# Kernel optimization log

Hardware: AMD Instinct MI355X
Metric: run time of the kernel (lower is better)

Reference implementation:

```python
import jax, jax.numpy as jnp
import numpy as np

N, E, C, MID = 20000, 320000, 16, 32
EPS = 1e-8

# ---- real Clebsch-Gordan (Q_J) matrices for degree pairs up to l=1, real-SH m-order (-l..l) i.e. (y,z,x) for l=1 ----

def _q_matrices():
    Q0 = np.eye(3, dtype=np.float32)[:, :, None] / np.sqrt(3.0)          # 1x1 -> J=0
    eps = np.zeros((3, 3, 3), dtype=np.float32)
    for (a, b, c_) in [(0, 1, 2), (1, 2, 0), (2, 0, 1)]:
        eps[a, b, c_] = 1.0
        eps[a, c_, b] = -1.0
    Q1 = eps / np.sqrt(2.0)                                               # 1x1 -> J=1 (cross product)
    Q2 = np.zeros((3, 3, 5), dtype=np.float32)                            # 1x1 -> J=2 (sym traceless)
    s2 = 1.0 / np.sqrt(2.0); s6 = 1.0 / np.sqrt(6.0)
    Q2[2, 0, 0] = Q2[0, 2, 0] = s2          # ~xy
    Q2[0, 1, 1] = Q2[1, 0, 1] = s2          # ~yz
    Q2[0, 0, 2] = -s6; Q2[1, 1, 2] = 2 * s6; Q2[2, 2, 2] = -s6  # ~(2z2-x2-y2)
    Q2[1, 2, 3] = Q2[2, 1, 3] = s2          # ~xz
    Q2[2, 2, 4] = s2; Q2[0, 0, 4] = -s2     # ~(x2-y2)
    return Q0, Q1, Q2

_Q0, _Q1, _Q2 = _q_matrices()


def _basis(u):
    """u: [E,3] unit edge directions -> basis tensors per (d_in,d_out) pair."""
    x, y, z = u[:, 0], u[:, 1], u[:, 2]
    Ep = u.shape[0]
    Y0 = jnp.full((Ep,), 0.28209479177387814, u.dtype)
    Y1 = 0.4886025119029199 * jnp.stack([y, z, x], -1)                    # m=-1,0,1
    Y2 = jnp.stack([1.0925484305920792 * x * y,
                    1.0925484305920792 * y * z,
                    0.31539156525252005 * (3.0 * z * z - 1.0),
                    1.0925484305920792 * x * z,
                    0.5462742152960396 * (x * x - y * y)], -1)
    b00 = Y0.reshape(Ep, 1, 1, 1, 1, 1)
    b01 = Y1.reshape(Ep, 1, 3, 1, 1, 1)
    b10 = Y1.reshape(Ep, 1, 1, 1, 3, 1)
    K0 = Y0[:, None, None] * jnp.asarray(_Q0[:, :, 0])
    K1 = jnp.einsum('em,abm->eab', Y1, jnp.asarray(_Q1))
    K2 = jnp.einsum('em,abm->eab', Y2, jnp.asarray(_Q2))
    b11 = jnp.stack([K0, K1, K2], -1).reshape(Ep, 1, 3, 1, 3, 3)          # num_freq=3 (J=0,1,2)
    return b00, b01, b10, b11


def _bn(x, g, b):  # BatchNorm1d, training-mode stats over edges, eps=1e-5
    mu = x.mean(0)
    var = ((x - mu) ** 2).mean(0)
    return (x - mu) * jax.lax.rsqrt(var + 1e-5) * g + b


def _hidden(feat, W1, b1, g1, be1, W2, b2, g2, be2):
    h = jax.nn.relu(_bn(feat @ W1 + b1, g1, be1))
    return jax.nn.relu(_bn(h @ W2 + b2, g2, be2))


def _kernel(Rflat, basis, nco, do_dim, nci, di_dim, nf):
    # RadialFunc output view: [E, nc_out, 1, nc_in, 1, num_freq]; contract freq with basis
    R = Rflat.reshape(-1, nco, 1, nci, 1, nf)
    k = (R * basis).sum(-1)                        # [E,nco,do_dim,nci,di_dim]
    return k.reshape(-1, nco * do_dim, nci * di_dim)


def _norm_bias(x, bias):  # GNormBias: relu(|x| + b) * phase
    n = jnp.sqrt((x * x).sum(-1, keepdims=True) + 1e-12)
    phase = x / jnp.maximum(n, EPS)
    return jax.nn.relu(n[..., 0] + bias)[..., None] * phase


def _forward(src, dst, pos, c, v, w,
             rW1, rb1, rg1, rbe1, rW2, rb2, rg2, rbe2,
             w3_a00, b3_a00, w3_a01, b3_a01, w3_a10, b3_a10, w3_a11, b3_a11,
             w3_b01, b3_b01, w3_b11, b3_b11,
             selfA0, selfA1, selfB1, nbias0, nbias1):
    n_nodes = c.shape[0]
    n_edges = src.shape[0]
    rel = pos[dst] - pos[src]
    r = jnp.sqrt((rel * rel).sum(-1, keepdims=True))                      # [E,1]
    u = rel / jnp.maximum(r, EPS)
    b00, b01, b10, b11 = _basis(u)
    feat = jnp.concatenate([w, r], -1)                                    # [E, edge_dim+1]
    # all 6 radial-net hiddens at once: [6,E,MID]
    H = jax.vmap(_hidden, in_axes=(None, 0, 0, 0, 0, 0, 0, 0, 0))(
        feat, rW1, rb1, rg1, rbe1, rW2, rb2, rg2, rbe2)
    deg = jax.ops.segment_sum(jnp.ones((n_edges,), feat.dtype), dst, num_segments=n_nodes)
    inv = (1.0 / jnp.maximum(deg, 1.0))[:, None, None]
    mask = (deg > 0).astype(feat.dtype)[:, None, None]
    # ---- layer A: in {0:1,1:1} -> mid {0:C,1:C} ----
    k00 = _kernel(H[0] @ w3_a00 + b3_a00, b00, C, 1, 1, 1, 1)             # [E,C,1]
    k01 = _kernel(H[1] @ w3_a01 + b3_a01, b01, C, 3, 1, 1, 1)             # [E,3C,1]
    k10 = _kernel(H[2] @ w3_a10 + b3_a10, b10, C, 1, 1, 3, 1)             # [E,C,3]
    k11 = _kernel(H[3] @ w3_a11 + b3_a11, b11, C, 3, 1, 3, 3)             # [E,3C,3]
    s0 = c[src].reshape(n_edges, 1, 1)
    s1 = v[src].reshape(n_edges, 3, 1)
    m0 = (k00 @ s0 + k10 @ s1).reshape(n_edges, C, 1)
    m1 = (k01 @ s0 + k11 @ s1).reshape(n_edges, C, 3)
    h0 = jax.ops.segment_sum(m0, dst, num_segments=n_nodes) * inv \
         + jnp.einsum('oi,nid->nod', selfA0[0], c) * mask
    h1 = jax.ops.segment_sum(m1, dst, num_segments=n_nodes) * inv \
         + jnp.einsum('oi,nid->nod', selfA1[0], v) * mask
    # ---- GNormBias on mid fiber ----
    h0 = _norm_bias(h0, nbias0)
    h1 = _norm_bias(h1, nbias1)
    # ---- layer B: mid {0:C,1:C} -> out {1:2} ----
    kb01 = _kernel(H[4] @ w3_b01 + b3_b01, b01, 2, 3, C, 1, 1)            # [E,6,C]
    kb11 = _kernel(H[5] @ w3_b11 + b3_b11, b11, 2, 3, C, 3, 3)            # [E,6,3C]
    t0 = h0[src]                                                          # [E,C,1]
    t1 = h1[src].reshape(n_edges, C * 3, 1)
    mB = (kb01 @ t0 + kb11 @ t1).reshape(n_edges, 2, 3)
    out = jax.ops.segment_sum(mB, dst, num_segments=n_nodes) * inv \
          + jnp.einsum('oi,nid->nod', selfB1[0], h1) * mask
    return out                                                            # [N,2,3]


def setup_inputs() -> dict:
    key = jax.random.key(0)
    ks = jax.random.split(key, 40)
    def rn(i, shape, scale=1.0):
        return jax.random.normal(ks[i], shape, jnp.float32) * scale
    K = 6
    sc = 1.0 / np.sqrt(MID)
    d = {}
    d['src'] = jax.random.randint(ks[0], (E,), 0, N)
    d['dst'] = jax.random.randint(ks[1], (E,), 0, N)
    d['pos'] = rn(2, (N, 3))
    d['c'] = rn(3, (N, 1, 1))
    d['v'] = rn(4, (N, 1, 3))
    d['w'] = rn(5, (E, 1))
    d['rW1'] = rn(6, (K, 2, MID), 1.0 / np.sqrt(2.0))
    d['rb1'] = jnp.zeros((K, MID), jnp.float32)
    d['rg1'] = jnp.ones((K, MID), jnp.float32)
    d['rbe1'] = jnp.zeros((K, MID), jnp.float32)
    d['rW2'] = rn(7, (K, MID, MID), sc)
    d['rb2'] = jnp.zeros((K, MID), jnp.float32)
    d['rg2'] = jnp.ones((K, MID), jnp.float32)
    d['rbe2'] = jnp.zeros((K, MID), jnp.float32)
    d['w3_a00'] = rn(8, (MID, C), sc);      d['b3_a00'] = jnp.zeros((C,), jnp.float32)
    d['w3_a01'] = rn(9, (MID, C), sc);      d['b3_a01'] = jnp.zeros((C,), jnp.float32)
    d['w3_a10'] = rn(10, (MID, C), sc);     d['b3_a10'] = jnp.zeros((C,), jnp.float32)
    d['w3_a11'] = rn(11, (MID, 3 * C), sc); d['b3_a11'] = jnp.zeros((3 * C,), jnp.float32)
    d['w3_b01'] = rn(12, (MID, 2 * C), sc); d['b3_b01'] = jnp.zeros((2 * C,), jnp.float32)
    d['w3_b11'] = rn(13, (MID, 6 * C), sc); d['b3_b11'] = jnp.zeros((6 * C,), jnp.float32)
    d['selfA0'] = rn(14, (1, C, 1))
    d['selfA1'] = rn(15, (1, C, 1))
    d['selfB1'] = rn(16, (1, 2, C), 1.0 / np.sqrt(C))
    d['nbias0'] = rn(17, (C,))
    d['nbias1'] = rn(18, (C,))
    return d


def reference(src, dst, pos, c, v, w,
              rW1, rb1, rg1, rbe1, rW2, rb2, rg2, rbe2,
              w3_a00, b3_a00, w3_a01, b3_a01, w3_a10, b3_a10, w3_a11, b3_a11,
              w3_b01, b3_b01, w3_b11, b3_b11,
              selfA0, selfA1, selfB1, nbias0, nbias1):
    return _forward(src, dst, pos, c, v, w,
                    rW1, rb1, rg1, rbe1, rW2, rb2, rg2, rbe2,
                    w3_a00, b3_a00, w3_a01, b3_a01, w3_a10, b3_a10, w3_a11, b3_a11,
                    w3_b01, b3_b01, w3_b11, b3_b11,
                    selfA0, selfA1, selfB1, nbias0, nbias1)
```

## Files before the change

### kernel.cpp

```cpp
#include <hip/hip_runtime.h>

#define NN 20000
#define NE 320000
#define CDIM 16
#define MID 32
#define EPSF 1e-8f

#define SCHED_FENCE() __builtin_amdgcn_sched_barrier(0)

#define OFF_DEGI   848
#define ZERO_WORDS 20848
#define OFF_ROWPTR 20848
#define OFF_CURSOR 40864
#define OFF_EORDER 60864
#define OFF_SRCS   380864
#define OFF_WSRT   700864
#define OFF_FW1A   1020864
#define OFF_FW1B   1021056
#define OFF_FC1    1021248
#define OFF_BN2A   1021440
#define OFF_FC2    1021632
#define OFF_FW2T   1021824
#define OFF_ECS    1027968
#define OFF_H0N    2307968
#define OFF_H1N    2627968
#define OFF_MSGA0  3587968
#define OFF_MSGA1  8707968
#define OFF_MSGB   24067968

#define Y0C   0.28209479177387814f
#define Y1C   0.4886025119029199f
#define Y2C1  1.0925484305920792f
#define Y2C2  0.31539156525252005f
#define Y2C3  0.5462742152960396f
#define S2C   0.7071067811865476f
#define S6C   0.4082482904638631f
#define K0C   0.16286750396763996f

__device__ __forceinline__ void atomAddD(double* p, double v) {
  unsafeAtomicAdd(p, v);
}

__device__ __forceinline__ void mlpH_lds(
    const float* __restrict__ a1, const float* __restrict__ b1v,
    const float* __restrict__ c1, const float* __restrict__ c2,
    const float* __restrict__ W2T, float we, float r, float* H) {
  float h[MID];
#pragma unroll
  for (int j4 = 0; j4 < 8; ++j4) {
    float4 av = ((const float4*)a1)[j4];
    float4 bv = ((const float4*)b1v)[j4];
    float4 cv = ((const float4*)c1)[j4];
    h[4 * j4 + 0] = fmaxf(fmaf(we, av.x, fmaf(r, bv.x, cv.x)), 0.0f);
    h[4 * j4 + 1] = fmaxf(fmaf(we, av.y, fmaf(r, bv.y, cv.y)), 0.0f);
    h[4 * j4 + 2] = fmaxf(fmaf(we, av.z, fmaf(r, bv.z, cv.z)), 0.0f);
    h[4 * j4 + 3] = fmaxf(fmaf(we, av.w, fmaf(r, bv.w, cv.w)), 0.0f);
  }
  SCHED_FENCE();
#pragma unroll
  for (int jg = 0; jg < 8; ++jg) {
#pragma unroll
    for (int jq = 0; jq < 4; ++jq) {
      const int j = jg * 4 + jq;
      float acc = c2[j];
      const float4* wp = (const float4*)(W2T + j * MID);
#pragma unroll
      for (int i4 = 0; i4 < 8; ++i4) {
        float4 wv = wp[i4];
        acc = fmaf(h[4 * i4 + 0], wv.x, acc);
        acc = fmaf(h[4 * i4 + 1], wv.y, acc);
        acc = fmaf(h[4 * i4 + 2], wv.z, acc);
        acc = fmaf(h[4 * i4 + 3], wv.w, acc);
      }
// ... 29 lines not shown
  for (int jg = 0; jg < 8; ++jg) {
#pragma unroll
    for (int jq = 0; jq < 4; ++jq) {
      const int j = jg * 4 + jq;
      float c2v = c2[j];
      float accA = c2v, accB = c2v;
      const float4* wp = (const float4*)(W2T + j * MID);
#pragma unroll
      for (int i4 = 0; i4 < 8; ++i4) {
        float4 wv = wp[i4];
        accA = fmaf(hA[4 * i4 + 0], wv.x, accA);
        accB = fmaf(hB[4 * i4 + 0], wv.x, accB);
        accA = fmaf(hA[4 * i4 + 1], wv.y, accA);
        accB = fmaf(hB[4 * i4 + 1], wv.y, accB);
        accA = fmaf(hA[4 * i4 + 2], wv.z, accA);
        accB = fmaf(hB[4 * i4 + 2], wv.z, accB);
        accA = fmaf(hA[4 * i4 + 3], wv.w, accA);
        accB = fmaf(hB[4 * i4 + 3], wv.w, accB);
      }
      HA[j] = fmaxf(accA, 0.0f);
      HB[j] = fmaxf(accB, 0.0f);
    }
    SCHED_FENCE();
  }
}

__global__ __launch_bounds__(256) void k_hist(
    const int* __restrict__ dst, float* __restrict__ ws) {
  int e = blockIdx.x * blockDim.x + threadIdx.x;
  if (e >= NE) return;
  atomicAdd((int*)ws + OFF_DEGI + dst[e], 1);
}

__global__ void k_scan(float* __restrict__ ws) {
  __shared__ int buf[256];
  __shared__ int carry;
  const int* degi = (const int*)ws + OFF_DEGI;
  int* rowptr = (int*)ws + OFF_ROWPTR;
  int* cursor = (int*)ws + OFF_CURSOR;
  int tid = threadIdx.x;
  if (tid == 0) carry = 0;
  __syncthreads();
  for (int base = 0; base < NN; base += 256) {
    int v = (base + tid < NN) ? degi[base + tid] : 0;
    buf[tid] = v;
    __syncthreads();
    for (int off = 1; off < 256; off <<= 1) {
      int t = buf[tid];
      int add = (tid >= off) ? buf[tid - off] : 0;
      __syncthreads();
      buf[tid] = t + add;
      __syncthreads();
    }
    int excl = buf[tid] - v;
    if (base + tid < NN) {
      rowptr[base + tid] = carry + excl;
      cursor[base + tid] = carry + excl;
    }
    __syncthreads();
    if (tid == 255) carry += buf[255];
    __syncthreads();
  }
  if (tid == 0) rowptr[NN] = carry;
}

__global__ __launch_bounds__(256) void k_scatter(
    const int* __restrict__ dst, float* __restrict__ ws) {
  int e = blockIdx.x * blockDim.x + threadIdx.x;
  if (e >= NE) return;
  int* cursor = (int*)ws + OFF_CURSOR;
  int* eorder = (int*)ws + OFF_EORDER;
  int d = dst[e];
  int p = atomicAdd(cursor + d, 1);
  eorder[p] = e;
}

__global__ __launch_bounds__(256) void k_geo(
    const int* __restrict__ src, const int* __restrict__ dst,
    const float* __restrict__ pos, const float* __restrict__ w,
    float* __restrict__ ws) {
  __shared__ double sred[20];
  double lw = 0, lr = 0, lww = 0, lrr = 0, lwr = 0;
  const int* eorder = (const int*)ws + OFF_EORDER;
  int* srcs = (int*)ws + OFF_SRCS;
  float* wsrt = ws + OFF_WSRT;
  float4* ecs = (float4*)(ws + OFF_ECS);
  for (int t = blockIdx.x * blockDim.x + threadIdx.x; t < NE;
       t += gridDim.x * blockDim.x) {
    int e = eorder[t];
    int s = src[e], d = dst[e];
    float dx = pos[3 * d + 0] - pos[3 * s + 0];
    float dy = pos[3 * d + 1] - pos[3 * s + 1];
    float dz = pos[3 * d + 2] - pos[3 * s + 2];
    float r = sqrtf(dx * dx + dy * dy + dz * dz);
    float ri = 1.0f / fmaxf(r, EPSF);
    ecs[t] = make_float4(r, dx * ri, dy * ri, dz * ri);
    float we = w[e];
    wsrt[t] = we;
    srcs[t] = s;
    double wd = (double)we, rd = (double)r;
    lw += wd; lr += rd; lww += wd * wd; lrr += rd * rd; lwr += wd * rd;
  }
#pragma unroll
  for (int d = 32; d >= 1; d >>= 1) {
    lw += __shfl_xor(lw, d);
    lr += __shfl_xor(lr, d);
    lww += __shfl_xor(lww, d);
    lrr += __shfl_xor(lrr, d);
    lwr += __shfl_xor(lwr, d);
  }
  int wid = threadIdx.x >> 6;
  if ((threadIdx.x & 63) == 0) {
    sred[0 * 4 + wid] = lw;
    sred[1 * 4 + wid] = lr;
    sred[2 * 4 + wid] = lww;
    sred[3 * 4 + wid] = lrr;
    sred[4 * 4 + wid] = lwr;
  }
  __syncthreads();
  if (threadIdx.x < 5) {
    double v = sred[threadIdx.x * 4 + 0] + sred[threadIdx.x * 4 + 1]
             + sred[threadIdx.x * 4 + 2] + sred[threadIdx.x * 4 + 3];
    atomAddD((double*)ws + threadIdx.x * 8, v);
  }
}

__global__ void k_fin1(const float* __restrict__ rW1, const float* __restrict__ rb1,
                       const float* __restrict__ rg1, const float* __restrict__ rbe1,
                       float* __restrict__ ws) {
  int t = threadIdx.x;
  int k = t >> 5, j = t & 31;
  const double* s1 = (const double*)ws;
  double Sw = s1[0], Sr = s1[8], Sww = s1[16], Srr = s1[24], Swr = s1[32];
  const double inv = 1.0 / (double)NE;
  double W0 = (double)rW1[k * 64 + j], W1 = (double)rW1[k * 64 + 32 + j];
  double b = (double)rb1[k * 32 + j];
  double mlin = (Sw * W0 + Sr * W1) * inv;
  double mu = mlin + b;
  double ex2 = (Sww * W0 * W0 + Srr * W1 * W1 + 2.0 * Swr * W0 * W1) * inv
             + 2.0 * b * mlin + b * b;
  double var = ex2 - mu * mu;
  double a = (double)rg1[k * 32 + j] / sqrt(var + 1e-5);
  ws[OFF_FW1A + t] = (float)(W0 * a);
  ws[OFF_FW1B + t] = (float)(W1 * a);
  ws[OFF_FC1 + t] = (float)((double)rbe1[k * 32 + j] - mlin * a);
}

__global__ __launch_bounds__(256) void k_stats2(
    const float* __restrict__ rW2, const float* __restrict__ rb2,
    float* __restrict__ ws) {
  const int k = blockIdx.y;
  const int j0 = blockIdx.z * 16;
  __shared__ __align__(16) float sW1a[32], sW1b[32], sc1[32];
  __shared__ __align__(16) float sW2c[512];
  __shared__ float sb2[16];
  __shared__ float sredf[2][16][4];
  int tid = threadIdx.x;
  if (tid < 32) {
    sW1a[tid] = ws[OFF_FW1A + k * 32 + tid];
    sW1b[tid] = ws[OFF_FW1B + k * 32 + tid];
    sc1[tid] = ws[OFF_FC1 + k * 32 + tid];
  }
  if (tid < 16) sb2[tid] = rb2[k * 32 + j0 + tid];
  for (int t = tid; t < 512; t += 256) {
    int jj = t >> 5, i = t & 31;
    sW2c[t] = rW2[k * 1024 + i * 32 + j0 + jj];
  }
  __syncthreads();
  const float4* ecs = (const float4*)(ws + OFF_ECS);
  const float* wsrt = ws + OFF_WSRT;
  float lsum[16], lsq[16];
#pragma unroll
  for (int jj = 0; jj < 16; ++jj) { lsum[jj] = 0.0f; lsq[jj] = 0.0f; }
  const int NP = NE / 2;
  for (int p = blockIdx.x * blockDim.x + tid; p < NP;
       p += gridDim.x * blockDim.x) {
    int e0 = 2 * p;
    float r0 = ecs[e0].x, r1 = ecs[e0 + 1].x;
    float w0 = wsrt[e0], w1 = wsrt[e0 + 1];
    float h0[MID], h1[MID];
#pragma unroll
    for (int j4 = 0; j4 < 8; ++j4) {
      float4 av = ((const float4*)sW1a)[j4];
      float4 bv = ((const float4*)sW1b)[j4];
      float4 cv = ((const float4*)sc1)[j4];
      h0[4 * j4 + 0] = fmaxf(fmaf(w0, av.x, fmaf(r0, bv.x, cv.x)), 0.0f);
      h1[4 * j4 + 0] = fmaxf(fmaf(w1, av.x, fmaf(r1, bv.x, cv.x)), 0.0f);
      h0[4 * j4 + 1] = fmaxf(fmaf(w0, av.y, fmaf(r0, bv.y, cv.y)), 0.0f);
      h1[4 * j4 + 1] = fmaxf(fmaf(w1, av.y, fmaf(r1, bv.y, cv.y)), 0.0f);
      h0[4 * j4 + 2] = fmaxf(fmaf(w0, av.z, fmaf(r0, bv.z, cv.z)), 0.0f);
      h1[4 * j4 + 2] = fmaxf(fmaf(w1, av.z, fmaf(r1, bv.z, cv.z)), 0.0f);
      h0[4 * j4 + 3] = fmaxf(fmaf(w0, av.w, fmaf(r0, bv.w, cv.w)), 0.0f);
      h1[4 * j4 + 3] = fmaxf(fmaf(w1, av.w, fmaf(r1, bv.w, cv.w)), 0.0f);
    }
    SCHED_FENCE();
#pragma unroll
    for (int jg = 0; jg < 4; ++jg) {
#pragma unroll
      for (int jq = 0; jq < 4; ++jq) {
        const int jj = jg * 4 + jq;
        float aE0 = sb2[jj], aE1 = sb2[jj];
        const float4* wp = (const float4*)(sW2c + jj * 32);
#pragma unroll
        for (int i4 = 0; i4 < 8; ++i4) {
          float4 wv = wp[i4];
          aE0 = fmaf(h0[4 * i4 + 0], wv.x, aE0);
          aE1 = fmaf(h1[4 * i4 + 0], wv.x, aE1);
          aE0 = fmaf(h0[4 * i4 + 1], wv.y, aE0);
          aE1 = fmaf(h1[4 * i4 + 1], wv.y, aE1);
          aE0 = fmaf(h0[4 * i4 + 2], wv.z, aE0);
          aE1 = fmaf(h1[4 * i4 + 2], wv.z, aE1);
          aE0 = fmaf(h0[4 * i4 + 3], wv.w, aE0);
// ... 24 lines not shown
    int jj = tid & 15, which = tid >> 4;
    float v = sredf[which][jj][0] + sredf[which][jj][1]
            + sredf[which][jj][2] + sredf[which][jj][3];
    double* s2 = (double*)(ws + 80);
    atomAddD(s2 + k * 64 + which * 32 + j0 + jj, (double)v);
  }
}

__global__ void k_fin2(const float* __restrict__ rb2,
                       const float* __restrict__ rg2, const float* __restrict__ rbe2,
                       float* __restrict__ ws) {
  int t = threadIdx.x;
  int k = t >> 5, j = t & 31;
  const double* s2 = (const double*)(ws + 80);
  const double inv = 1.0 / (double)NE;
  double mu = s2[k * 64 + j] * inv;
  double ex2 = s2[k * 64 + 32 + j] * inv;
  double var = ex2 - mu * mu;
  double a = (double)rg2[t] / sqrt(var + 1e-5);
  ws[OFF_BN2A + t] = (float)a;
  ws[OFF_FC2 + t] = (float)((double)rbe2[t] + ((double)rb2[t] - mu) * a);
}

__global__ __launch_bounds__(256) void k_fold2(const float* __restrict__ rW2,
                                               float* __restrict__ ws) {
  int idx = blockIdx.x * blockDim.x + threadIdx.x;
  if (idx >= 6144) return;
  int k = idx >> 10, rem = idx & 1023;
  int j = rem >> 5, i = rem & 31;
  ws[OFF_FW2T + idx] = rW2[k * 1024 + i * 32 + j] * ws[OFF_BN2A + k * 32 + j];
}

__global__ __launch_bounds__(256) void k_passA0(
    const float* __restrict__ cI, const float* __restrict__ vI,
    const float* __restrict__ w00, const float* __restrict__ b00,
    const float* __restrict__ w10, const float* __restrict__ b10,
    float* __restrict__ ws) {
  __shared__ __align__(16) float sW1a[64], sW1b[64], sc1[64], sc2[64];
  __shared__ __align__(16) float sW2T[2048];
  __shared__ __align__(16) float sP00[512], sP10[512];
  __shared__ float sB00[16], sB10[16];
  int tid = threadIdx.x;
  if (tid < 32) {
    sW1a[tid] = ws[OFF_FW1A + tid];       sW1a[32 + tid] = ws[OFF_FW1A + 64 + tid];
    sW1b[tid] = ws[OFF_FW1B + tid];       sW1b[32 + tid] = ws[OFF_FW1B + 64 + tid];
    sc1[tid]  = ws[OFF_FC1 + tid];        sc1[32 + tid]  = ws[OFF_FC1 + 64 + tid];
    sc2[tid]  = ws[OFF_FC2 + tid];        sc2[32 + tid]  = ws[OFF_FC2 + 64 + tid];
  }
  for (int t = tid; t < 2048; t += 256) {
    sW2T[t] = ws[OFF_FW2T + ((t < 1024) ? t : (1024 + t))];
  }
  for (int t = tid; t < 512; t += 256) {
    int i = t >> 4, co = t & 15;
    sP00[co * 32 + i] = w00[t];
    sP10[co * 32 + i] = w10[t];
  }
  if (tid < 16) { sB00[tid] = b00[tid]; sB10[tid] = b10[tid]; }
  __syncthreads();

  const int* srcs = (const int*)ws + OFF_SRCS;
  const float* wsrt = ws + OFF_WSRT;
  const float4* ecs = (const float4*)(ws + OFF_ECS);
  int t = blockIdx.x * blockDim.x + tid;
  if (t >= NE) return;
  int s = srcs[t];
  float4 E = ecs[t];
  float we = wsrt[t];
  float cs = cI[s];
  float v0 = vI[3 * s + 0], v1 = vI[3 * s + 1], v2 = vI[3 * s + 2];
  float dY1v = Y1C * (E.z * v0 + E.w * v1 + E.y * v2);

  float H[MID], m0[CDIM];
  mlpH_lds(sW1a, sW1b, sc1, sc2, sW2T, we, E.x, H);
  float f0 = Y0C * cs;
#pragma unroll
  for (int cg = 0; cg < 4; ++cg) {
#pragma unroll
    for (int cq = 0; cq < 4; ++cq) {
      const int co = cg * 4 + cq;
      float a = sB00[co];
      const float4* wp = (const float4*)(sP00 + co * 32);
#pragma unroll
      for (int i4 = 0; i4 < 8; ++i4) {
        float4 wv = wp[i4];
        a = fmaf(H[4 * i4 + 0], wv.x, a);
        a = fmaf(H[4 * i4 + 1], wv.y, a);
        a = fmaf(H[4 * i4 + 2], wv.z, a);
        a = fmaf(H[4 * i4 + 3], wv.w, a);
      }
      m0[co] = a * f0;
    }
    SCHED_FENCE();
  }
  mlpH_lds(sW1a + 32, sW1b + 32, sc1 + 32, sc2 + 32, sW2T + 1024, we, E.x, H);
#pragma unroll
  for (int cg = 0; cg < 4; ++cg) {
#pragma unroll
    for (int cq = 0; cq < 4; ++cq) {
      const int co = cg * 4 + cq;
      float a = sB10[co];
      const float4* wp = (const float4*)(sP10 + co * 32);
#pragma unroll
      for (int i4 = 0; i4 < 8; ++i4) {
        float4 wv = wp[i4];
        a = fmaf(H[4 * i4 + 0], wv.x, a);
        a = fmaf(H[4 * i4 + 1], wv.y, a);
        a = fmaf(H[4 * i4 + 2], wv.z, a);
        a = fmaf(H[4 * i4 + 3], wv.w, a);
      }
      m0[co] = fmaf(a, dY1v, m0[co]);
    }
    SCHED_FENCE();
  }
  float4* mp = (float4*)(ws + OFF_MSGA0) + t * 4;
#pragma unroll
  for (int q = 0; q < 4; ++q)
    mp[q] = make_float4(m0[4 * q], m0[4 * q + 1], m0[4 * q + 2], m0[4 * q + 3]);
}

__global__ __launch_bounds__(256) void k_passA1(
    const float* __restrict__ cI, const float* __restrict__ vI,
    const float* __restrict__ w01, const float* __restrict__ b01,
    const float* __restrict__ w11, const float* __restrict__ b11,
    float* __restrict__ ws) {
  __shared__ __align__(16) float sW1a[64], sW1b[64], sc1[64], sc2[64];
  __shared__ __align__(16) float sW2T[2048];
  __shared__ __align__(16) float sP01[512], sP11[1536];
  __shared__ float sB01[16], sB11[48];
  int tid = threadIdx.x;
  if (tid < 32) {
    sW1a[tid] = ws[OFF_FW1A + 32 + tid];  sW1a[32 + tid] = ws[OFF_FW1A + 96 + tid];
    sW1b[tid] = ws[OFF_FW1B + 32 + tid];  sW1b[32 + tid] = ws[OFF_FW1B + 96 + tid];
    sc1[tid]  = ws[OFF_FC1 + 32 + tid];   sc1[32 + tid]  = ws[OFF_FC1 + 96 + tid];
    sc2[tid]  = ws[OFF_FC2 + 32 + tid];   sc2[32 + tid]  = ws[OFF_FC2 + 96 + tid];
  }
  for (int t = tid; t < 1024; t += 256) {
    sW2T[t] = ws[OFF_FW2T + 1024 + t];
    sW2T[1024 + t] = ws[OFF_FW2T + 3072 + t];
  }
  for (int t = tid; t < 512; t += 256) {
    int i = t >> 4, co = t & 15;
    sP01[co * 32 + i] = w01[t];
  }
  for (int t = tid; t < 1536; t += 256) {
    int i = t / 48, c = t - i * 48;
    sP11[c * 32 + i] = w11[t];
  }
  if (tid < 16) sB01[tid] = b01[tid];
  if (tid < 48) sB11[tid] = b11[tid];
  __syncthreads();

  const int* srcs = (const int*)ws + OFF_SRCS;
  const float* wsrt = ws + OFF_WSRT;
  const float4* ecs = (const float4*)(ws + OFF_ECS);
  int t = blockIdx.x * blockDim.x + tid;
  if (t >= NE) return;
  int s = srcs[t];
  float4 E = ecs[t];
  float we = wsrt[t];
  float cs = cI[s];

  float H[MID];
  float ra[16];
  mlpH_lds(sW1a, sW1b, sc1, sc2, sW2T, we, E.x, H);
#pragma unroll
  for (int cg = 0; cg < 4; ++cg) {
#pragma unroll
    for (int cq = 0; cq < 4; ++cq) {
      const int co = cg * 4 + cq;
      float a = sB01[co];
      const float4* wp = (const float4*)(sP01 + co * 32);
#pragma unroll
      for (int i4 = 0; i4 < 8; ++i4) {
        float4 wv = wp[i4];
        a = fmaf(H[4 * i4 + 0], wv.x, a);
        a = fmaf(H[4 * i4 + 1], wv.y, a);
        a = fmaf(H[4 * i4 + 2], wv.z, a);
        a = fmaf(H[4 * i4 + 3], wv.w, a);
      }
      ra[co] = a;
    }
    SCHED_FENCE();
  }
  mlpH_lds(sW1a + 32, sW1b + 32, sc1 + 32, sc2 + 32, sW2T + 1024, we, E.x, H);
  float y10 = Y1C * E.z, y11 = Y1C * E.w, y12 = Y1C * E.y;
  float KV[3][3];
  {
    float ux = E.y, uy = E.z, uz = E.w;
    float y20 = Y2C1 * ux * uy, y21 = Y2C1 * uy * uz;
    float y22 = Y2C2 * (3.0f * uz * uz - 1.0f);
    float y23 = Y2C1 * ux * uz, y24 = Y2C3 * (ux * ux - uy * uy);
    float S00 = -S6C * y22 - S2C * y24;
    float S11 = 2.0f * S6C * y22;
    float S22 = -S6C * y22 + S2C * y24;
    float S01 = S2C * y21, S02 = S2C * y20, S12 = S2C * y23;
    float v0 = vI[3 * s + 0], v1 = vI[3 * s + 1], v2 = vI[3 * s + 2];
    KV[0][0] = K0C * v0; KV[0][1] = K0C * v1; KV[0][2] = K0C * v2;
    KV[1][0] = S2C * (y12 * v1 - y11 * v2);
    KV[1][1] = S2C * (y10 * v2 - y12 * v0);
    KV[1][2] = S2C * (y11 * v0 - y10 * v1);
    KV[2][0] = S00 * v0 + S01 * v1 + S02 * v2;
    KV[2][1] = S01 * v0 + S11 * v1 + S12 * v2;
    KV[2][2] = S02 * v0 + S12 * v1 + S22 * v2;
  }
  float cy0 = cs * y10, cy1 = cs * y11, cy2 = cs * y12;
#pragma unroll 1
  for (int g = 0; g < 4; ++g) {
    float a[12];
#pragma unroll
    for (int q = 0; q < 4; ++q) {
      int co = g * 4 + q;
      float R0 = sB11[co * 3 + 0], R1 = sB11[co * 3 + 1], R2 = sB11[co * 3 + 2];
      const float4* p0 = (const float4*)(sP11 + (co * 3 + 0) * 32);
      const float4* p1 = (const float4*)(sP11 + (co * 3 + 1) * 32);
      const float4* p2 = (const float4*)(sP11 + (co * 3 + 2) * 32);
#pragma unroll
      for (int i4 = 0; i4 < 8; ++i4) {
        float4 w0v = p0[i4], w1v = p1[i4], w2v = p2[i4];
        float h0 = H[4 * i4 + 0], h1 = H[4 * i4 + 1];
        float h2 = H[4 * i4 + 2], h3 = H[4 * i4 + 3];
        R0 = fmaf(h0, w0v.x, R0); R1 = fmaf(h0, w1v.x, R1); R2 = fmaf(h0, w2v.x, R2);
        R0 = fmaf(h1, w0v.y, R0); R1 = fmaf(h1, w1v.y, R1); R2 = fmaf(h1, w2v.y, R2);
        R0 = fmaf(h2, w0v.z, R0); R1 = fmaf(h2, w1v.z, R1); R2 = fmaf(h2, w2v.z, R2);
        R0 = fmaf(h3, w0v.w, R0); R1 = fmaf(h3, w1v.w, R1); R2 = fmaf(h3, w2v.w, R2);
      }
      float r_ = ra[co];
      a[q * 3 + 0] = fmaf(r_, cy0, R0 * KV[0][0] + R1 * KV[1][0] + R2 * KV[2][0]);
      a[q * 3 + 1] = fmaf(r_, cy1, R0 * KV[0][1] + R1 * KV[1][1] + R2 * KV[2][1]);
      a[q * 3 + 2] = fmaf(r_, cy2, R0 * KV[0][2] + R1 * KV[1][2] + R2 * KV[2][2]);
    }
    float4* mp = (float4*)(ws + OFF_MSGA1 + g * (NE * 12)) + t * 3;
    mp[0] = make_float4(a[0], a[1], a[2], a[3]);
    mp[1] = make_float4(a[4], a[5], a[6], a[7]);
    mp[2] = make_float4(a[8], a[9], a[10], a[11]);
    SCHED_FENCE();
  }
}

__global__ __launch_bounds__(256) void k_nodeA(
    const float* __restrict__ cI, const float* __restrict__ vI,
    const float* __restrict__ selfA0, const float* __restrict__ selfA1,
    const float* __restrict__ nbias0, const float* __restrict__ nbias1,
    float* __restrict__ ws) {
  int idx = blockIdx.x * blockDim.x + threadIdx.x;
  if (idx >= NN * CDIM) return;
  int n = idx >> 4, co = idx & 15;
  const int* rowptr = (const int*)ws + OFF_ROWPTR;
  int r0 = rowptr[n], r1 = rowptr[n + 1];
  const float* mA0 = ws + OFF_MSGA0;
  const float* mA1 = ws + OFF_MSGA1 + (co >> 2) * (NE * 12) + (co & 3) * 3;
  float x0 = 0.0f, xa = 0.0f, xb = 0.0f, xc = 0.0f;
  for (int row = r0; row < r1; ++row) {
    x0 += mA0[row * 16 + co];
    xa += mA1[row * 12 + 0];
    xb += mA1[row * 12 + 1];
    xc += mA1[row * 12 + 2];
  }
  float dg = (float)(r1 - r0);
  float iv = 1.0f / fmaxf(dg, 1.0f);
  float mk = dg > 0.0f ? 1.0f : 0.0f;
  x0 = x0 * iv + selfA0[co] * cI[n] * mk;
  float n0 = sqrtf(x0 * x0 + 1e-12f);
  ws[OFF_H0N + idx] = fmaxf(n0 + nbias0[co], 0.0f) * (x0 / fmaxf(n0, EPSF));
  xa = xa * iv + selfA1[co] * vI[3 * n + 0] * mk;
  xb = xb * iv + selfA1[co] * vI[3 * n + 1] * mk;
  xc = xc * iv + selfA1[co] * vI[3 * n + 2] * mk;
  float nv = sqrtf(xa * xa + xb * xb + xc * xc + 1e-12f);
  float sc = fmaxf(nv + nbias1[co], 0.0f) / fmaxf(nv, EPSF);
  ws[OFF_H1N + idx * 3 + 0] = xa * sc;
  ws[OFF_H1N + idx * 3 + 1] = xb * sc;
  ws[OFF_H1N + idx * 3 + 2] = xc * sc;
}

__global__ __launch_bounds__(256) void k_passB(
    const float* __restrict__ wb01, const float* __restrict__ bb01,
    const float* __restrict__ wb11, const float* __restrict__ bb11,
    float* __restrict__ ws) {
  __shared__ __align__(16) float sW1a[64], sW1b[64], sc1[64], sc2[64];
  __shared__ __align__(16) float sW2T[2048];
  __shared__ __align__(16) float sPB01[1024];
  __shared__ __align__(16) float sPB11[3072];
  __shared__ float sBB01[32];
  __shared__ float sBB11[96];
  int tid = threadIdx.x;
  if (tid < 64) {
    sW1a[tid] = ws[OFF_FW1A + 128 + tid];
    sW1b[tid] = ws[OFF_FW1B + 128 + tid];
    sc1[tid] = ws[OFF_FC1 + 128 + tid];
    sc2[tid] = ws[OFF_FC2 + 128 + tid];
  }
  for (int t = tid; t < 2048; t += 256) sW2T[t] = ws[OFF_FW2T + 4096 + t];
  for (int t = tid; t < 1024; t += 256) {
    int i = t >> 5, c = t & 31;
    int o = c >> 4, ci = c & 15;
    sPB01[(ci * 2 + o) * 32 + i] = wb01[t];
  }
  for (int t = tid; t < 3072; t += 256) {
    int i = t / 96, c = t - i * 96;
    int o = c / 48, rem = c - o * 48;
    int ci = rem / 3, f = rem - ci * 3;
    sPB11[(ci * 6 + o * 3 + f) * 32 + i] = wb11[t];
  }
  if (tid < 32) {
    int o = tid >> 4, ci = tid & 15;
    sBB01[ci * 2 + o] = bb01[tid];
  }
  if (tid < 96) {
    int o = tid / 48, rem = tid - o * 48;
    int ci = rem / 3, f = rem - ci * 3;
    sBB11[ci * 6 + o * 3 + f] = bb11[tid];
  }
  __syncthreads();

  const int* srcs = (const int*)ws + OFF_SRCS;
  const float* wsrt = ws + OFF_WSRT;
  const float4* ecs = (const float4*)(ws + OFF_ECS);
  const int NP = NE / 2;
  int p = blockIdx.x * blockDim.x + tid;
  if (p >= NP) return;
  {
    int tA = 2 * p, tB = 2 * p + 1;
    int sA = srcs[tA], sB_ = srcs[tB];
    float4 EA = ecs[tA], EB = ecs[tB];
    float weA = wsrt[tA], weB = wsrt[tB];

    float HA[MID], HB[MID];
    mlpH2_lds(sW1a, sW1b, sc1, sc2, sW2T, weA, EA.x, weB, EB.x, HA, HB);
    const float* h0pA = ws + OFF_H0N + sA * CDIM;
    const float* h0pB = ws + OFF_H0N + sB_ * CDIM;
    float A0A = 0.0f, A1A = 0.0f, A0B = 0.0f, A1B = 0.0f;
#pragma unroll 1
    for (int ci = 0; ci < CDIM; ++ci) {
      float bA = h0pA[ci], bB = h0pB[ci];
      float R0A = sBB01[ci * 2 + 0], R1A = sBB01[ci * 2 + 1];
      float R0B = R0A, R1B = R1A;
      const float4* p0 = (const float4*)(sPB01 + (ci * 2 + 0) * 32);
      const float4* p1 = (const float4*)(sPB01 + (ci * 2 + 1) * 32);
#pragma unroll
      for (int i4 = 0; i4 < 8; ++i4) {
        float4 w0v = p0[i4], w1v = p1[i4];
        float hA0 = HA[4 * i4 + 0], hB0 = HB[4 * i4 + 0];
        float hA1 = HA[4 * i4 + 1], hB1 = HB[4 * i4 + 1];
        float hA2 = HA[4 * i4 + 2], hB2 = HB[4 * i4 + 2];
        float hA3 = HA[4 * i4 + 3], hB3 = HB[4 * i4 + 3];
        R0A = fmaf(hA0, w0v.x, R0A); R0B = fmaf(hB0, w0v.x, R0B);
        R1A = fmaf(hA0, w1v.x, R1A); R1B = fmaf(hB0, w1v.x, R1B);
        R0A = fmaf(hA1, w0v.y, R0A); R0B = fmaf(hB1, w0v.y, R0B);
        R1A = fmaf(hA1, w1v.y, R1A); R1B = fmaf(hB1, w1v.y, R1B);
        R0A = fmaf(hA2, w0v.z, R0A); R0B = fmaf(hB2, w0v.z, R0B);
        R1A = fmaf(hA2, w1v.z, R1A); R1B = fmaf(hB2, w1v.z, R1B);
        R0A = fmaf(hA3, w0v.w, R0A); R0B = fmaf(hB3, w0v.w, R0B);
        R1A = fmaf(hA3, w1v.w, R1A); R1B = fmaf(hB3, w1v.w, R1B);
      }
      A0A = fmaf(R0A, bA, A0A); A1A = fmaf(R1A, bA, A1A);
      A0B = fmaf(R0B, bB, A0B); A1B = fmaf(R1B, bB, A1B);
      SCHED_FENCE();
    }
// ... 17 lines not shown
        float RB = RA;
        const float4* wp = (const float4*)(sPB11 + (ci * 6 + of) * 32);
#pragma unroll
        for (int i4 = 0; i4 < 8; ++i4) {
          float4 wv = wp[i4];
          RA = fmaf(HA[4 * i4 + 0], wv.x, RA);
          RB = fmaf(HB[4 * i4 + 0], wv.x, RB);
          RA = fmaf(HA[4 * i4 + 1], wv.y, RA);
          RB = fmaf(HB[4 * i4 + 1], wv.y, RB);
          RA = fmaf(HA[4 * i4 + 2], wv.z, RA);
          RB = fmaf(HB[4 * i4 + 2], wv.z, RB);
          RA = fmaf(HA[4 * i4 + 3], wv.w, RA);
          RB = fmaf(HB[4 * i4 + 3], wv.w, RB);
        }
        GA[of][0] = fmaf(RA, bA0, GA[of][0]);
        GA[of][1] = fmaf(RA, bA1, GA[of][1]);
        GA[of][2] = fmaf(RA, bA2, GA[of][2]);
        GB[of][0] = fmaf(RB, bB0, GB[of][0]);
        GB[of][1] = fmaf(RB, bB1, GB[of][1]);
        GB[of][2] = fmaf(RB, bB2, GB[of][2]);
      }
      SCHED_FENCE();
    }
    {
      float ux = EA.y, uy = EA.z, uz = EA.w;
      float y10 = Y1C * uy, y11 = Y1C * uz, y12 = Y1C * ux;
      float y20 = Y2C1 * ux * uy, y21 = Y2C1 * uy * uz;
      float y22 = Y2C2 * (3.0f * uz * uz - 1.0f);
      float y23 = Y2C1 * ux * uz, y24 = Y2C3 * (ux * ux - uy * uy);
      float S00 = -S6C * y22 - S2C * y24;
      float S11 = 2.0f * S6C * y22;
      float S22 = -S6C * y22 + S2C * y24;
      float S01 = S2C * y21, S02 = S2C * y20, S12 = S2C * y23;
      float4* mp = (float4*)(ws + OFF_MSGB) + tA * 2;
#pragma unroll
      for (int o = 0; o < 2; ++o) {
        float Ao = (o == 0) ? A0A : A1A;
        float m0 = Ao * y10 + K0C * GA[o * 3 + 0][0]
                 + S2C * (y12 * GA[o * 3 + 1][1] - y11 * GA[o * 3 + 1][2])
                 + S00 * GA[o * 3 + 2][0] + S01 * GA[o * 3 + 2][1] + S02 * GA[o * 3 + 2][2];
        float m1 = Ao * y11 + K0C * GA[o * 3 + 0][1]
                 + S2C * (y10 * GA[o * 3 + 1][2] - y12 * GA[o * 3 + 1][0])
                 + S01 * GA[o * 3 + 2][0] + S11 * GA[o * 3 + 2][1] + S12 * GA[o * 3 + 2][2];
        float m2 = Ao * y12 + K0C * GA[o * 3 + 0][2]
                 + S2C * (y11 * GA[o * 3 + 1][0] - y10 * GA[o * 3 + 1][1])
                 + S02 * GA[o * 3 + 2][0] + S12 * GA[o * 3 + 2][1] + S22 * GA[o * 3 + 2][2];
        mp[o] = make_float4(m0, m1, m2, 0.0f);
      }
    }
    {
      float ux = EB.y, uy = EB.z, uz = EB.w;
      float y10 = Y1C * uy, y11 = Y1C * uz, y12 = Y1C * ux;
      float y20 = Y2C1 * ux * uy, y21 = Y2C1 * uy * uz;
      float y22 = Y2C2 * (3.0f * uz * uz - 1.0f);
      float y23 = Y2C1 * ux * uz, y24 = Y2C3 * (ux * ux - uy * uy);
      float S00 = -S6C * y22 - S2C * y24;
      float S11 = 2.0f * S6C * y22;
      float S22 = -S6C * y22 + S2C * y24;
      float S01 = S2C * y21, S02 = S2C * y20, S12 = S2C * y23;
      float4* mp = (float4*)(ws + OFF_MSGB) + tB * 2;
#pragma unroll
      for (int o = 0; o < 2; ++o) {
        float Ao = (o == 0) ? A0B : A1B;
        float m0 = Ao * y10 + K0C * GB[o * 3 + 0][0]
                 + S2C * (y12 * GB[o * 3 + 1][1] - y11 * GB[o * 3 + 1][2])
                 + S00 * GB[o * 3 + 2][0] + S01 * GB[o * 3 + 2][1] + S02 * GB[o * 3 + 2][2];
        float m1 = Ao * y11 + K0C * GB[o * 3 + 0][1]
                 + S2C * (y10 * GB[o * 3 + 1][2] - y12 * GB[o * 3 + 1][0])
                 + S01 * GB[o * 3 + 2][0] + S11 * GB[o * 3 + 2][1] + S12 * GB[o * 3 + 2][2];
        float m2 = Ao * y12 + K0C * GB[o * 3 + 0][2]
                 + S2C * (y11 * GB[o * 3 + 1][0] - y10 * GB[o * 3 + 1][1])
                 + S02 * GB[o * 3 + 2][0] + S12 * GB[o * 3 + 2][1] + S22 * GB[o * 3 + 2][2];
        mp[o] = make_float4(m0, m1, m2, 0.0f);
      }
    }
  }
}

__global__ __launch_bounds__(256) void k_nodeB(
    const float* __restrict__ selfB1, float* __restrict__ out,
    const float* __restrict__ ws) {
  int idx = blockIdx.x * blockDim.x + threadIdx.x;
  if (idx >= NN * 6) return;
  int n = idx / 6;
  int q = idx - n * 6;
  int o = q / 3, a = q - o * 3;
  const int* rowptr = (const int*)ws + OFF_ROWPTR;
  int r0 = rowptr[n], r1 = rowptr[n + 1];
  const float* msgB = ws + OFF_MSGB;
  int col = o * 4 + a;
  float sum = 0.0f;
  for (int row = r0; row < r1; ++row) sum += msgB[row * 8 + col];
  float dg = (float)(r1 - r0);
  float iv = 1.0f / fmaxf(dg, 1.0f);
  float mk = dg > 0.0f ? 1.0f : 0.0f;
  const float* h1p = ws + OFF_H1N + n * CDIM * 3;
  float self = 0.0f;
#pragma unroll
  for (int ci = 0; ci < CDIM; ++ci)
    self = fmaf(selfB1[o * CDIM + ci], h1p[ci * 3 + a], self);
  out[idx] = sum * iv + self * mk;
}

extern "C" void kernel_launch(void* const* d_in, const int* in_sizes, int n_in,
                              void* d_out, int out_size, void* d_ws, size_t ws_size,
                              hipStream_t stream) {
  (void)in_sizes; (void)n_in; (void)out_size; (void)ws_size;
  const int* src = (const int*)d_in[0];
  const int* dst = (const int*)d_in[1];
  const float* pos = (const float*)d_in[2];
  const float* cI = (const float*)d_in[3];
  const float* vI = (const float*)d_in[4];
  const float* w = (const float*)d_in[5];
  const float* rW1 = (const float*)d_in[6];
  const float* rb1 = (const float*)d_in[7];
  const float* rg1 = (const float*)d_in[8];
  const float* rbe1 = (const float*)d_in[9];
  const float* rW2 = (const float*)d_in[10];
  const float* rb2 = (const float*)d_in[11];
  const float* rg2 = (const float*)d_in[12];
  const float* rbe2 = (const float*)d_in[13];
  const float* w3_a00 = (const float*)d_in[14];
  const float* b3_a00 = (const float*)d_in[15];
  const float* w3_a01 = (const float*)d_in[16];
  const float* b3_a01 = (const float*)d_in[17];
  const float* w3_a10 = (const float*)d_in[18];
  const float* b3_a10 = (const float*)d_in[19];
  const float* w3_a11 = (const float*)d_in[20];
  const float* b3_a11 = (const float*)d_in[21];
  const float* w3_b01 = (const float*)d_in[22];
  const float* b3_b01 = (const float*)d_in[23];
  const float* w3_b11 = (const float*)d_in[24];
  const float* b3_b11 = (const float*)d_in[25];
  const float* selfA0 = (const float*)d_in[26];
  const float* selfA1 = (const float*)d_in[27];
  const float* selfB1 = (const float*)d_in[28];
  const float* nbias0 = (const float*)d_in[29];
  const float* nbias1 = (const float*)d_in[30];
  float* ws = (float*)d_ws;
  float* out = (float*)d_out;

  hipMemsetAsync(d_ws, 0, (size_t)ZERO_WORDS * 4, stream);

  k_hist<<<1250, 256, 0, stream>>>(dst, ws);
  k_scan<<<1, 256, 0, stream>>>(ws);
  k_scatter<<<1250, 256, 0, stream>>>(dst, ws);
  k_geo<<<1250, 256, 0, stream>>>(src, dst, pos, w, ws);
  k_fin1<<<1, 192, 0, stream>>>(rW1, rb1, rg1, rbe1, ws);
  k_stats2<<<dim3(256, 6, 2), 256, 0, stream>>>(rW2, rb2, ws);
  k_fin2<<<1, 192, 0, stream>>>(rb2, rg2, rbe2, ws);
  k_fold2<<<24, 256, 0, stream>>>(rW2, ws);
  k_passA0<<<1250, 256, 0, stream>>>(cI, vI, w3_a00, b3_a00, w3_a10, b3_a10, ws);
  k_passA1<<<1250, 256, 0, stream>>>(cI, vI, w3_a01, b3_a01, w3_a11, b3_a11, ws);
  k_nodeA<<<1250, 256, 0, stream>>>(cI, vI, selfA0, selfA1, nbias0, nbias1, ws);
  k_passB<<<625, 256, 0, stream>>>(w3_b01, b3_b01, w3_b11, b3_b11, ws);
  k_nodeB<<<469, 256, 0, stream>>>(selfB1, out, ws);
}
```

Baseline: 540.2 us.

## Replace CSR sort and per-edge message buffers with atomic scatter-add into node accumulators

Drops the scan and scatter kernels that sorted edges by destination, along with the per-edge message arrays that the node kernels later gathered over CSR rows. Edge kernels now read src, dst and w directly in original order and atomically add their messages into per-node float accumulators, which the node kernels read directly. This removes two launches, the permutation traffic and large intermediate writes. In exchange it adds many float atomics, contended on high-degree nodes, a larger memset, and a nondeterministic summation order.

Result: slower. 1.480 ms (+173.9%).

```diff
diff --git a/kernel.cpp b/kernel.cpp
--- a/kernel.cpp
+++ b/kernel.cpp
@@ -9,24 +9,19 @@
 #define SCHED_FENCE() __builtin_amdgcn_sched_barrier(0)
 
 #define OFF_DEGI   848
-#define ZERO_WORDS 20848
-#define OFF_ROWPTR 20848
-#define OFF_CURSOR 40864
-#define OFF_EORDER 60864
-#define OFF_SRCS   380864
-#define OFF_WSRT   700864
-#define OFF_FW1A   1020864
-#define OFF_FW1B   1021056
-#define OFF_FC1    1021248
-#define OFF_BN2A   1021440
-#define OFF_FC2    1021632
-#define OFF_FW2T   1021824
-#define OFF_ECS    1027968
-#define OFF_H0N    2307968
-#define OFF_H1N    2627968
-#define OFF_MSGA0  3587968
-#define OFF_MSGA1  8707968
-#define OFF_MSGB   24067968
+#define OFF_ACCA0  20848
+#define OFF_ACCA1  340848
+#define OFF_ACCB   1300848
+#define ZERO_WORDS 1420848
+#define OFF_FW1A   1420848
+#define OFF_FW1B   1421040
+#define OFF_FC1    1421232
+#define OFF_BN2A   1421424
+#define OFF_FC2    1421616
+#define OFF_FW2T   1421808
+#define OFF_ECS    1427952
+#define OFF_H0N    2707952
+#define OFF_H1N    3027952
 
 #define Y0C   0.28209479177387814f
 #define Y1C   0.4886025119029199f
@@ -39,6 +34,9 @@
 
 __device__ __forceinline__ void atomAddD(double* p, double v) {
   unsafeAtomicAdd(p, v);
+}
+__device__ __forceinline__ void atomAddF(float* p, float v) {
+  atomicAdd(p, v);
 }
 
 __device__ __forceinline__ void mlpH_lds(
@@ -134,72 +132,23 @@
   atomicAdd((int*)ws + OFF_DEGI + dst[e], 1);
 }
 
-__global__ void k_scan(float* __restrict__ ws) {
-  __shared__ int buf[256];
-  __shared__ int carry;
-  const int* degi = (const int*)ws + OFF_DEGI;
-  int* rowptr = (int*)ws + OFF_ROWPTR;
-  int* cursor = (int*)ws + OFF_CURSOR;
-  int tid = threadIdx.x;
-  if (tid == 0) carry = 0;
-  __syncthreads();
-  for (int base = 0; base < NN; base += 256) {
-    int v = (base + tid < NN) ? degi[base + tid] : 0;
-    buf[tid] = v;
-    __syncthreads();
-    for (int off = 1; off < 256; off <<= 1) {
-      int t = buf[tid];
-      int add = (tid >= off) ? buf[tid - off] : 0;
-      __syncthreads();
-      buf[tid] = t + add;
-      __syncthreads();
-    }
-    int excl = buf[tid] - v;
-    if (base + tid < NN) {
-      rowptr[base + tid] = carry + excl;
-      cursor[base + tid] = carry + excl;
-    }
-    __syncthreads();
-    if (tid == 255) carry += buf[255];
-    __syncthreads();
-  }
-  if (tid == 0) rowptr[NN] = carry;
-}
-
-__global__ __launch_bounds__(256) void k_scatter(
-    const int* __restrict__ dst, float* __restrict__ ws) {
-  int e = blockIdx.x * blockDim.x + threadIdx.x;
-  if (e >= NE) return;
-  int* cursor = (int*)ws + OFF_CURSOR;
-  int* eorder = (int*)ws + OFF_EORDER;
-  int d = dst[e];
-  int p = atomicAdd(cursor + d, 1);
-  eorder[p] = e;
-}
-
 __global__ __launch_bounds__(256) void k_geo(
     const int* __restrict__ src, const int* __restrict__ dst,
     const float* __restrict__ pos, const float* __restrict__ w,
     float* __restrict__ ws) {
   __shared__ double sred[20];
   double lw = 0, lr = 0, lww = 0, lrr = 0, lwr = 0;
-  const int* eorder = (const int*)ws + OFF_EORDER;
-  int* srcs = (int*)ws + OFF_SRCS;
-  float* wsrt = ws + OFF_WSRT;
   float4* ecs = (float4*)(ws + OFF_ECS);
-  for (int t = blockIdx.x * blockDim.x + threadIdx.x; t < NE;
-       t += gridDim.x * blockDim.x) {
-    int e = eorder[t];
+  for (int e = blockIdx.x * blockDim.x + threadIdx.x; e < NE;
+       e += gridDim.x * blockDim.x) {
     int s = src[e], d = dst[e];
     float dx = pos[3 * d + 0] - pos[3 * s + 0];
     float dy = pos[3 * d + 1] - pos[3 * s + 1];
     float dz = pos[3 * d + 2] - pos[3 * s + 2];
     float r = sqrtf(dx * dx + dy * dy + dz * dz);
     float ri = 1.0f / fmaxf(r, EPSF);
-    ecs[t] = make_float4(r, dx * ri, dy * ri, dz * ri);
+    ecs[e] = make_float4(r, dx * ri, dy * ri, dz * ri);
     float we = w[e];
-    wsrt[t] = we;
-    srcs[t] = s;
     double wd = (double)we, rd = (double)r;
     lw += wd; lr += rd; lww += wd * wd; lrr += rd * rd; lwr += wd * rd;
   }
@@ -250,7 +199,7 @@
 
 __global__ __launch_bounds__(256) void k_stats2(
     const float* __restrict__ rW2, const float* __restrict__ rb2,
-    float* __restrict__ ws) {
+    const float* __restrict__ w, float* __restrict__ ws) {
   const int k = blockIdx.y;
   const int j0 = blockIdx.z * 16;
   __shared__ __align__(16) float sW1a[32], sW1b[32], sc1[32];
@@ -270,7 +219,6 @@
   }
   __syncthreads();
   const float4* ecs = (const float4*)(ws + OFF_ECS);
-  const float* wsrt = ws + OFF_WSRT;
   float lsum[16], lsq[16];
 #pragma unroll
   for (int jj = 0; jj < 16; ++jj) { lsum[jj] = 0.0f; lsq[jj] = 0.0f; }
@@ -279,7 +227,7 @@
        p += gridDim.x * blockDim.x) {
     int e0 = 2 * p;
     float r0 = ecs[e0].x, r1 = ecs[e0 + 1].x;
-    float w0 = wsrt[e0], w1 = wsrt[e0 + 1];
+    float w0 = w[e0], w1 = w[e0 + 1];
     float h0[MID], h1[MID];
 #pragma unroll
     for (int j4 = 0; j4 < 8; ++j4) {
@@ -370,6 +318,8 @@
 }
 
 __global__ __launch_bounds__(256) void k_passA0(
+    const int* __restrict__ src, const int* __restrict__ dst,
+    const float* __restrict__ wE,
     const float* __restrict__ cI, const float* __restrict__ vI,
     const float* __restrict__ w00, const float* __restrict__ b00,
     const float* __restrict__ w10, const float* __restrict__ b10,
@@ -396,14 +346,12 @@
   if (tid < 16) { sB00[tid] = b00[tid]; sB10[tid] = b10[tid]; }
   __syncthreads();
 
-  const int* srcs = (const int*)ws + OFF_SRCS;
-  const float* wsrt = ws + OFF_WSRT;
   const float4* ecs = (const float4*)(ws + OFF_ECS);
   int t = blockIdx.x * blockDim.x + tid;
   if (t >= NE) return;
-  int s = srcs[t];
+  int s = src[t], d = dst[t];
   float4 E = ecs[t];
-  float we = wsrt[t];
+  float we = wE[t];
   float cs = cI[s];
   float v0 = vI[3 * s + 0], v1 = vI[3 * s + 1], v2 = vI[3 * s + 2];
   float dY1v = Y1C * (E.z * v0 + E.w * v1 + E.y * v2);
@@ -450,13 +398,14 @@
     }
     SCHED_FENCE();
   }
-  float4* mp = (float4*)(ws + OFF_MSGA0) + t * 4;
-#pragma unroll
-  for (int q = 0; q < 4; ++q)
-    mp[q] = make_float4(m0[4 * q], m0[4 * q + 1], m0[4 * q + 2], m0[4 * q + 3]);
+  float* acc = ws + OFF_ACCA0 + (size_t)d * 16;
+#pragma unroll
+  for (int co = 0; co < 16; ++co) atomAddF(acc + co, m0[co]);
 }
 
 __global__ __launch_bounds__(256) void k_passA1(
+    const int* __restrict__ src, const int* __restrict__ dst,
+    const float* __restrict__ wE,
     const float* __restrict__ cI, const float* __restrict__ vI,
     const float* __restrict__ w01, const float* __restrict__ b01,
     const float* __restrict__ w11, const float* __restrict__ b11,
@@ -488,14 +437,12 @@
   if (tid < 48) sB11[tid] = b11[tid];
   __syncthreads();
 
-  const int* srcs = (const int*)ws + OFF_SRCS;
-  const float* wsrt = ws + OFF_WSRT;
   const float4* ecs = (const float4*)(ws + OFF_ECS);
   int t = blockIdx.x * blockDim.x + tid;
   if (t >= NE) return;
-  int s = srcs[t];
+  int s = src[t], d = dst[t];
   float4 E = ecs[t];
-  float we = wsrt[t];
+  float we = wE[t];
   float cs = cI[s];
 
   float H[MID];
@@ -542,6 +489,7 @@
     KV[2][2] = S02 * v0 + S12 * v1 + S22 * v2;
   }
   float cy0 = cs * y10, cy1 = cs * y11, cy2 = cs * y12;
+  float* accb = ws + OFF_ACCA1 + (size_t)d * 48;
 #pragma unroll 1
   for (int g = 0; g < 4; ++g) {
     float a[12];
@@ -567,10 +515,9 @@
       a[q * 3 + 1] = fmaf(r_, cy1, R0 * KV[0][1] + R1 * KV[1][1] + R2 * KV[2][1]);
       a[q * 3 + 2] = fmaf(r_, cy2, R0 * KV[0][2] + R1 * KV[1][2] + R2 * KV[2][2]);
     }
-    float4* mp = (float4*)(ws + OFF_MSGA1 + g * (NE * 12)) + t * 3;
-    mp[0] = make_float4(a[0], a[1], a[2], a[3]);
-    mp[1] = make_float4(a[4], a[5], a[6], a[7]);
-    mp[2] = make_float4(a[8], a[9], a[10], a[11]);
+    float* accg = accb + g * 12;
+#pragma unroll
+    for (int u = 0; u < 12; ++u) atomAddF(accg + u, a[u]);
     SCHED_FENCE();
   }
 }
@@ -583,23 +530,17 @@
   int idx = blockIdx.x * blockDim.x + threadIdx.x;
   if (idx >= NN * CDIM) return;
   int n = idx >> 4, co = idx & 15;
-  const int* rowptr = (const int*)ws + OFF_ROWPTR;
-  int r0 = rowptr[n], r1 = rowptr[n + 1];
-  const float* mA0 = ws + OFF_MSGA0;
-  const float* mA1 = ws + OFF_MSGA1 + (co >> 2) * (NE * 12) + (co & 3) * 3;
-  float x0 = 0.0f, xa = 0.0f, xb = 0.0f, xc = 0.0f;
-  for (int row = r0; row < r1; ++row) {
-    x0 += mA0[row * 16 + co];
-    xa += mA1[row * 12 + 0];
-    xb += mA1[row * 12 + 1];
-    xc += mA1[row * 12 + 2];
-  }
-  float dg = (float)(r1 - r0);
+  const int* degi = (const int*)ws + OFF_DEGI;
+  float dg = (float)degi[n];
   float iv = 1.0f / fmaxf(dg, 1.0f);
   float mk = dg > 0.0f ? 1.0f : 0.0f;
+  float x0 = ws[OFF_ACCA0 + idx];
   x0 = x0 * iv + selfA0[co] * cI[n] * mk;
   float n0 = sqrtf(x0 * x0 + 1e-12f);
   ws[OFF_H0N + idx] = fmaxf(n0 + nbias0[co], 0.0f) * (x0 / fmaxf(n0, EPSF));
+  float xa = ws[OFF_ACCA1 + idx * 3 + 0];
+  float xb = ws[OFF_ACCA1 + idx * 3 + 1];
+  float xc = ws[OFF_ACCA1 + idx * 3 + 2];
   xa = xa * iv + selfA1[co] * vI[3 * n + 0] * mk;
   xb = xb * iv + selfA1[co] * vI[3 * n + 1] * mk;
   xc = xc * iv + selfA1[co] * vI[3 * n + 2] * mk;
@@ -611,6 +552,8 @@
 }
 
 __global__ __launch_bounds__(256) void k_passB(
+    const int* __restrict__ src, const int* __restrict__ dst,
+    const float* __restrict__ wE,
     const float* __restrict__ wb01, const float* __restrict__ bb01,
     const float* __restrict__ wb11, const float* __restrict__ bb11,
     float* __restrict__ ws) {
@@ -650,17 +593,16 @@
   }
   __syncthreads();
 
-  const int* srcs = (const int*)ws + OFF_SRCS;
-  const float* wsrt = ws + OFF_WSRT;
   const float4* ecs = (const float4*)(ws + OFF_ECS);
   const int NP = NE / 2;
   int p = blockIdx.x * blockDim.x + tid;
   if (p >= NP) return;
   {
     int tA = 2 * p, tB = 2 * p + 1;
-    int sA = srcs[tA], sB_ = srcs[tB];
+    int sA = src[tA], sB_ = src[tB];
+    int dA = dst[tA], dB = dst[tB];
     float4 EA = ecs[tA], EB = ecs[tB];
-    float weA = wsrt[tA], weB = wsrt[tB];
+    float weA = wE[tA], weB = wE[tB];
 
     float HA[MID], HB[MID];
     mlpH2_lds(sW1a, sW1b, sc1, sc2, sW2T, weA, EA.x, weB, EB.x, HA, HB);
@@ -744,7 +686,7 @@
       float S11 = 2.0f * S6C * y22;
       float S22 = -S6C * y22 + S2C * y24;
       float S01 = S2C * y21, S02 = S2C * y20, S12 = S2C * y23;
-      float4* mp = (float4*)(ws + OFF_MSGB) + tA * 2;
+      float* acc = ws + OFF_ACCB + (size_t)dA * 6;
 #pragma unroll
       for (int o = 0; o < 2; ++o) {
         float Ao = (o == 0) ? A0A : A1A;
@@ -757,7 +699,9 @@
         float m2 = Ao * y12 + K0C * GA[o * 3 + 0][2]
                  + S2C * (y11 * GA[o * 3 + 1][0] - y10 * GA[o * 3 + 1][1])
                  + S02 * GA[o * 3 + 2][0] + S12 * GA[o * 3 + 2][1] + S22 * GA[o * 3 + 2][2];
-        mp[o] = make_float4(m0, m1, m2, 0.0f);
+        atomAddF(acc + o * 3 + 0, m0);
+        atomAddF(acc + o * 3 + 1, m1);
+        atomAddF(acc + o * 3 + 2, m2);
       }
     }
     {
@@ -770,7 +714,7 @@
       float S11 = 2.0f * S6C * y22;
       float S22 = -S6C * y22 + S2C * y24;
       float S01 = S2C * y21, S02 = S2C * y20, S12 = S2C * y23;
-      float4* mp = (float4*)(ws + OFF_MSGB) + tB * 2;
+      float* acc = ws + OFF_ACCB + (size_t)dB * 6;
 #pragma unroll
       for (int o = 0; o < 2; ++o) {
         float Ao = (o == 0) ? A0B : A1B;
@@ -783,7 +727,9 @@
         float m2 = Ao * y12 + K0C * GB[o * 3 + 0][2]
                  + S2C * (y11 * GB[o * 3 + 1][0] - y10 * GB[o * 3 + 1][1])
                  + S02 * GB[o * 3 + 2][0] + S12 * GB[o * 3 + 2][1] + S22 * GB[o * 3 + 2][2];
-        mp[o] = make_float4(m0, m1, m2, 0.0f);
+        atomAddF(acc + o * 3 + 0, m0);
+        atomAddF(acc + o * 3 + 1, m1);
+        atomAddF(acc + o * 3 + 2, m2);
       }
     }
   }
@@ -797,15 +743,11 @@
   int n = idx / 6;
   int q = idx - n * 6;
   int o = q / 3, a = q - o * 3;
-  const int* rowptr = (const int*)ws + OFF_ROWPTR;
-  int r0 = rowptr[n], r1 = rowptr[n + 1];
-  const float* msgB = ws + OFF_MSGB;
-  int col = o * 4 + a;
-  float sum = 0.0f;
-  for (int row = r0; row < r1; ++row) sum += msgB[row * 8 + col];
-  float dg = (float)(r1 - r0);
+  const int* degi = (const int*)ws + OFF_DEGI;
+  float dg = (float)degi[n];
   float iv = 1.0f / fmaxf(dg, 1.0f);
   float mk = dg > 0.0f ? 1.0f : 0.0f;
+  float sum = ws[OFF_ACCB + idx];
   const float* h1p = ws + OFF_H1N + n * CDIM * 3;
   float self = 0.0f;
 #pragma unroll
@@ -855,16 +797,16 @@
   hipMemsetAsync(d_ws, 0, (size_t)ZERO_WORDS * 4, stream);
 
   k_hist<<<1250, 256, 0, stream>>>(dst, ws);
-  k_scan<<<1, 256, 0, stream>>>(ws);
-  k_scatter<<<1250, 256, 0, stream>>>(dst, ws);
   k_geo<<<1250, 256, 0, stream>>>(src, dst, pos, w, ws);
   k_fin1<<<1, 192, 0, stream>>>(rW1, rb1, rg1, rbe1, ws);
-  k_stats2<<<dim3(256, 6, 2), 256, 0, stream>>>(rW2, rb2, ws);
+  k_stats2<<<dim3(256, 6, 2), 256, 0, stream>>>(rW2, rb2, w, ws);
   k_fin2<<<1, 192, 0, stream>>>(rb2, rg2, rbe2, ws);
   k_fold2<<<24, 256, 0, stream>>>(rW2, ws);
-  k_passA0<<<1250, 256, 0, stream>>>(cI, vI, w3_a00, b3_a00, w3_a10, b3_a10, ws);
-  k_passA1<<<1250, 256, 0, stream>>>(cI, vI, w3_a01, b3_a01, w3_a11, b3_a11, ws);
+  k_passA0<<<1250, 256, 0, stream>>>(src, dst, w, cI, vI, w3_a00, b3_a00,
+                                     w3_a10, b3_a10, ws);
+  k_passA1<<<1250, 256, 0, stream>>>(src, dst, w, cI, vI, w3_a01, b3_a01,
+                                     w3_a11, b3_a11, ws);
   k_nodeA<<<1250, 256, 0, stream>>>(cI, vI, selfA0, selfA1, nbias0, nbias1, ws);
-  k_passB<<<625, 256, 0, stream>>>(w3_b01, b3_b01, w3_b11, b3_b11, ws);
+  k_passB<<<625, 256, 0, stream>>>(src, dst, w, w3_b01, b3_b01, w3_b11, b3_b11, ws);
   k_nodeB<<<469, 256, 0, stream>>>(selfB1, out, ws);
 }
```
